# Optimization experiments

Hardware: AMD Instinct MI355X
Metric: run time of the kernel (lower is better)

The kernel has to match this reference:

```python
import jax, jax.numpy as jnp
import numpy as np

D_MODEL = 1024
HIDDEN = 2048            # hidden_dimension // num_smaller_experts_per_expert
E_ROUTED = 14            # total_num_experts*num_smaller - num_shared
E_SHARED = 2
TOP_K = 2                # num_activated*num_smaller - num_shared
EPS = 1e-9               # config.epsilon
RMS_EPS = 1.1920929e-07  # torch RMSNorm default eps=None -> finfo(float32).eps


def setup_inputs() -> dict:
    key = jax.random.key(0)
    ks = jax.random.split(key, 9)
    B, T = 2, 1024
    x = jax.random.normal(ks[0], (B, T, D_MODEL), dtype=jnp.float32)
    router_w = jax.random.normal(ks[1], (D_MODEL, E_ROUTED), dtype=jnp.float32) * 0.006
    rms_w = jnp.ones((E_ROUTED, D_MODEL), dtype=jnp.float32)
    w1 = jax.random.normal(ks[2], (E_ROUTED, D_MODEL, HIDDEN), dtype=jnp.float32) * 0.02
    w2 = jax.random.normal(ks[3], (E_ROUTED, HIDDEN, D_MODEL), dtype=jnp.float32) * 0.02
    rms_w_s = jnp.ones((E_SHARED, D_MODEL), dtype=jnp.float32)
    w1_s = jax.random.normal(ks[4], (E_SHARED, D_MODEL, HIDDEN), dtype=jnp.float32) * 0.02
    w2_s = jax.random.normal(ks[5], (E_SHARED, HIDDEN, D_MODEL), dtype=jnp.float32) * 0.02
    return {"x": x, "router_w": router_w, "rms_w": rms_w, "w1": w1, "w2": w2,
            "rms_w_s": rms_w_s, "w1_s": w1_s, "w2_s": w2_s}


def _ffn(xn, rw, W1, W2):
    # RMSNorm -> Linear -> SiLU -> Linear (dropout is identity in eval)
    ms = jnp.mean(xn * xn, axis=-1, keepdims=True)
    h = (xn * jax.lax.rsqrt(ms + RMS_EPS)) * rw
    return jax.nn.silu(h @ W1) @ W2


def reference(x, router_w, rms_w, w1, w2, rms_w_s, w1_s, w2_s):
    B, T, D = x.shape
    N = B * T
    xf = x.reshape(N, D)
    # router gates + top-k sparsification + renormalization
    gates = jax.nn.softmax(xf @ router_w, axis=-1)          # [N, E]
    top_v, top_i = jax.lax.top_k(gates, TOP_K)              # [N, K]
    masked = jnp.zeros_like(gates).at[jnp.arange(N)[:, None], top_i].set(top_v)
    masked = masked / (masked.sum(axis=-1, keepdims=True) + EPS)  # [N, E]
    # routed experts: compute each expert on all tokens, combine with sparse gate weights
    # (same math as dispatch/index_add combine since masked is 0 off the top-k)
    routed = jax.vmap(lambda rw_, W1_, W2_: _ffn(xf, rw_, W1_, W2_))(rms_w, w1, w2)  # [E, N, D]
    routed_out = jnp.einsum('end,ne->nd', routed, masked)
    # shared experts: unweighted sum
    shared = jax.vmap(lambda rw_, W1_, W2_: _ffn(xf, rw_, W1_, W2_))(rms_w_s, w1_s, w2_s).sum(0)
    return (routed_out + shared).reshape(B, T, D)
```

## Files before the change

kernel.cpp:

```cpp
#include <hip/hip_runtime.h>
#include <hip/hip_bf16.h>
#include <cstdint>
#include <cstddef>

#define D_MODEL 1024
#define HIDDEN 2048
#define E_ROUTED 14
#define E_TOT 16
#define NTOK 2048
#define NASSIGN 4096
#define NROWS 8192

typedef __bf16 bf16x8 __attribute__((ext_vector_type(8)));
typedef float f32x4 __attribute__((ext_vector_type(4)));

static __device__ __forceinline__ unsigned short f2b(float f) {
  unsigned int u = __builtin_bit_cast(unsigned int, f);
  u += 0x7fffu + ((u >> 16) & 1u);
  return (unsigned short)(u >> 16);
}

#define ASYNC_COPY16(gptr, lptr)                                                        \
  __builtin_amdgcn_global_load_lds(                                                     \
      (const __attribute__((address_space(1))) unsigned int*)(gptr),                    \
      (__attribute__((address_space(3))) unsigned int*)(lptr), 16, 0, 0)

__global__ __launch_bounds__(256) void router_kernel(
    const float* __restrict__ x, const float* __restrict__ rweight,
    int* __restrict__ topi, float* __restrict__ topw,
    unsigned short* __restrict__ xhat) {
  int n = blockIdx.x, tid = threadIdx.x;
  const float4 xv = reinterpret_cast<const float4*>(x + (size_t)n * D_MODEL)[tid];
  float ss = xv.x * xv.x + xv.y * xv.y + xv.z * xv.z + xv.w * xv.w;
  float lg[E_ROUTED];
#pragma unroll
  for (int e = 0; e < E_ROUTED; ++e) lg[e] = 0.f;
  const float xa[4] = {xv.x, xv.y, xv.z, xv.w};
#pragma unroll
  for (int i = 0; i < 4; ++i) {
    const float* rw = rweight + (size_t)(tid * 4 + i) * E_ROUTED;
    float xd = xa[i];
#pragma unroll
    for (int e = 0; e < E_ROUTED; ++e) lg[e] = fmaf(xd, rw[e], lg[e]);
  }
#pragma unroll
  for (int off = 32; off > 0; off >>= 1) {
    ss += __shfl_xor(ss, off);
#pragma unroll
    for (int e = 0; e < E_ROUTED; ++e) lg[e] += __shfl_xor(lg[e], off);
  }
  __shared__ float red[4][16];
  int wid = tid >> 6, lane = tid & 63;
  if (lane == 0) {
    red[wid][0] = ss;
#pragma unroll
    for (int e = 0; e < E_ROUTED; ++e) red[wid][1 + e] = lg[e];
  }
  __syncthreads();
  __shared__ float s_scale;
  if (tid == 0) {
    float fin[15];
    for (int v = 0; v < 15; ++v) fin[v] = red[0][v] + red[1][v] + red[2][v] + red[3][v];
    s_scale = rsqrtf(fin[0] * (1.f / D_MODEL) + 1.1920929e-07f);
    float mx = fin[1];
    for (int e = 1; e < E_ROUTED; ++e) mx = fmaxf(mx, fin[1 + e]);
    float p[E_ROUTED]; float Z = 0.f;
    for (int e = 0; e < E_ROUTED; ++e) { p[e] = __expf(fin[1 + e] - mx); Z += p[e]; }
    int i0 = 0; float v0 = p[0];
    for (int e = 1; e < E_ROUTED; ++e) if (p[e] > v0) { v0 = p[e]; i0 = e; }
    int i1 = (i0 == 0) ? 1 : 0; float v1 = p[i1];
    for (int e = 0; e < E_ROUTED; ++e) if (e != i0 && p[e] > v1) { v1 = p[e]; i1 = e; }
    v0 /= Z; v1 /= Z;
    float inv = 1.f / (v0 + v1 + 1e-9f);
    topi[2 * n] = i0; topi[2 * n + 1] = i1;
    topw[2 * n] = v0 * inv; topw[2 * n + 1] = v1 * inv;
  }
  __syncthreads();
  float sc = s_scale;
  ushort4 hx;
  hx.x = f2b(xv.x * sc); hx.y = f2b(xv.y * sc);
  hx.z = f2b(xv.z * sc); hx.w = f2b(xv.w * sc);
  reinterpret_cast<ushort4*>(xhat + (size_t)n * D_MODEL)[tid] = hx;
}

__global__ __launch_bounds__(256) void count_kernel(const int* __restrict__ topi,
                                                    int* __restrict__ goff,
                                                    int* __restrict__ cursor) {
  __shared__ int cnt[E_ROUTED];
  int tid = threadIdx.x;
  if (tid < E_ROUTED) cnt[tid] = 0;
  __syncthreads();
  for (int i = tid; i < NASSIGN; i += 256) atomicAdd(&cnt[topi[i]], 1);
  __syncthreads();
  if (tid == 0) {
    int acc = 0;
    for (int e = 0; e < E_ROUTED; ++e) { goff[e] = acc; cursor[e] = acc; acc += cnt[e]; }
    goff[E_ROUTED] = acc;
  }
}

__global__ __launch_bounds__(256) void scatter_kernel(
    const int* __restrict__ topi, const float* __restrict__ topw,
    int* __restrict__ cursor, int* __restrict__ row_token,
    float* __restrict__ row_gate, int* __restrict__ token_rows) {
  int i = blockIdx.x * 256 + threadIdx.x;
  if (i >= NASSIGN) return;
  int e = topi[i];
  int pos = atomicAdd(&cursor[e], 1);
  row_token[pos] = i >> 1;
  row_gate[pos] = topw[i];
  token_rows[i] = pos;
}

template <int K, int N, bool SCALE>
__global__ __launch_bounds__(256) void convT_kernel(
    const float* __restrict__ Wr, const float* __restrict__ Ws,
    const float* __restrict__ RWr, const float* __restrict__ RWs,
    unsigned short* __restrict__ outT) {
  __shared__ float tile[64][65];
  int g = blockIdx.z;
  const float* src = (g < E_ROUTED) ? Wr + (size_t)g * K * N
                                    : Ws + (size_t)(g - E_ROUTED) * K * N;
  const float* rw = nullptr;
  if constexpr (SCALE)
    rw = (g < E_ROUTED) ? RWr + (size_t)g * K : RWs + (size_t)(g - E_ROUTED) * K;
  int k0 = blockIdx.y * 64, nn0 = blockIdx.x * 64;
  int t = threadIdx.x;
  int kk = t >> 4, nc = (t & 15) * 4;
#pragma unroll
  for (int j = 0; j < 4; ++j) {
    int k = kk + j * 16;
    float4 v = *(const float4*)(src + (size_t)(k0 + k) * N + nn0 + nc);
    float s = 1.f;
    if constexpr (SCALE) s = rw[k0 + k];
    tile[k][nc]     = v.x * s;
    tile[k][nc + 1] = v.y * s;
    tile[k][nc + 2] = v.z * s;
    tile[k][nc + 3] = v.w * s;
  }
  __syncthreads();
  int k8 = (t & 7) * 8;
#pragma unroll
  for (int p = 0; p < 2; ++p) {
    int n = (t >> 3) + p * 32;
    uint4 pk;
    pk.x = (unsigned)f2b(tile[k8 + 0][n]) | ((unsigned)f2b(tile[k8 + 1][n]) << 16);
    pk.y = (unsigned)f2b(tile[k8 + 2][n]) | ((unsigned)f2b(tile[k8 + 3][n]) << 16);
    pk.z = (unsigned)f2b(tile[k8 + 4][n]) | ((unsigned)f2b(tile[k8 + 5][n]) << 16);
    pk.w = (unsigned)f2b(tile[k8 + 6][n]) | ((unsigned)f2b(tile[k8 + 7][n]) << 16);
    *(uint4*)(outT + ((size_t)g * N + nn0 + n) * K + k0 + k8) = pk;
  }
}

template <bool G1, int KTOT, int NTOT>
__global__ __launch_bounds__(256, 2) void ffn_gemm(
    const int* __restrict__ goff, const int* __restrict__ row_token,
    const float* __restrict__ row_gate,
    const unsigned short* __restrict__ Abase,
    const unsigned short* __restrict__ Wt,
    unsigned short* __restrict__ Hout, float* __restrict__ Yout) {
  int g = blockIdx.z;
  int grpStart, cnt;
  if (g < E_ROUTED) { grpStart = goff[g]; cnt = goff[g + 1] - goff[g]; }
  else { grpStart = NASSIGN + (g - E_ROUTED) * NTOK; cnt = NTOK; }
  int m0 = blockIdx.y * 128;
  if (m0 >= cnt) return;
  int n0 = blockIdx.x * 128;

  __shared__ __align__(16) char smem[2][32 * 1024];

  int tid = threadIdx.x, lane = tid & 63, wid = tid >> 6;
  int wr = (wid >> 1) * 64, wc = (wid & 1) * 64;
  int lrow = lane >> 3;
  int swz = lrow << 4;
  int colB = ((lane & 7) << 4) ^ swz;

  const char* aSrc[4];
  const char* bSrc[4];
#pragma unroll
  for (int i = 0; i < 4; ++i) {
    int row = wid * 32 + i * 8 + lrow;
    int rIdx = m0 + row; if (rIdx >= cnt) rIdx = cnt - 1;
    int srcRow;
    if constexpr (G1) srcRow = (g < E_ROUTED) ? row_token[grpStart + rIdx] : rIdx;
    else srcRow = grpStart + rIdx;
    aSrc[i] = (const char*)(Abase + (size_t)srcRow * KTOT) + colB;
    bSrc[i] = (const char*)(Wt + ((size_t)g * NTOT + n0 + row) * KTOT) + colB;
  }

  f32x4 acc[4][4];
#pragma unroll
  for (int m = 0; m < 4; ++m)
#pragma unroll
    for (int n = 0; n < 4; ++n)
#pragma unroll
      for (int c = 0; c < 4; ++c) acc[m][n][c] = 0.f;

  auto STAGE = [&](int buf) {
    char* sA = smem[buf];
    char* sB = smem[buf] + 16 * 1024;
#pragma unroll
    for (int i = 0; i < 4; ++i) ASYNC_COPY16(aSrc[i], sA + wid * 4096 + i * 1024);
#pragma unroll
    for (int i = 0; i < 4; ++i) ASYNC_COPY16(bSrc[i], sB + wid * 4096 + i * 1024);
#pragma unroll
    for (int i = 0; i < 4; ++i) { aSrc[i] += 128; bSrc[i] += 128; }
  };
  auto COMPUTE = [&](int buf) {
    const char* sA = smem[buf];
    const char* sB = smem[buf] + 16 * 1024;
#pragma unroll
    for (int ks = 0; ks < 2; ++ks) {
      int kb = ks * 64 + ((lane >> 4) << 4);
      bf16x8 af[4], bfr[4];
#pragma unroll
      for (int m = 0; m < 4; ++m) {
        int r = wr + m * 16 + (lane & 15);
        af[m] = *(const bf16x8*)(sA + (r << 7) + (kb ^ ((r & 7) << 4)));
      }
#pragma unroll
      for (int n = 0; n < 4; ++n) {
        int r = wc + n * 16 + (lane & 15);
        bfr[n] = *(const bf16x8*)(sB + (r << 7) + (kb ^ ((r & 7) << 4)));
      }
#pragma unroll
      for (int m = 0; m < 4; ++m)
#pragma unroll
        for (int n = 0; n < 4; ++n)
          acc[m][n] = __builtin_amdgcn_mfma_f32_16x16x32_bf16(af[m], bfr[n], acc[m][n], 0, 0, 0);
    }
  };

  constexpr int NT = KTOT / 64;
  STAGE(0);
  __syncthreads();
  for (int kt = 0; kt < NT; kt += 2) {
    STAGE(1);
    COMPUTE(0);
    __syncthreads();
    if (kt + 2 < NT) STAGE(0);
    COMPUTE(1);
    __syncthreads();
  }

  int lr = (lane >> 4) * 4, lc = lane & 15;
#pragma unroll
  for (int m = 0; m < 4; ++m) {
    int rloc = m0 + wr + m * 16 + lr;
#pragma unroll
    for (int j = 0; j < 4; ++j) {
      if (rloc + j < cnt) {
        size_t r = (size_t)(grpStart + rloc + j);
        if constexpr (G1) {
#pragma unroll
          for (int n = 0; n < 4; ++n) {
            float v = acc[m][n][j];
            float sv = v / (1.f + __expf(-v));
            Hout[r * HIDDEN + (n0 + wc + n * 16 + lc)] = f2b(sv);
          }
        } else {
          float gate = 1.f;
          if (g < E_ROUTED) gate = row_gate[r];
#pragma unroll
          for (int n = 0; n < 4; ++n)
            Yout[r * D_MODEL + (n0 + wc + n * 16 + lc)] = acc[m][n][j] * gate;
        }
      }
    }
  }
}

__global__ __launch_bounds__(256) void combine_kernel(
    const float* __restrict__ y, const int* __restrict__ token_rows,
    float* __restrict__ out) {
  int n = blockIdx.x, tid = threadIdx.x;
  int a0 = token_rows[2 * n], a1 = token_rows[2 * n + 1];
  const float4* y0 = reinterpret_cast<const float4*>(y + (size_t)a0 * D_MODEL);
  const float4* y1 = reinterpret_cast<const float4*>(y + (size_t)a1 * D_MODEL);
  const float4* s0 = reinterpret_cast<const float4*>(y + (size_t)(NASSIGN + n) * D_MODEL);
  const float4* s1 = reinterpret_cast<const float4*>(y + (size_t)(NASSIGN + NTOK + n) * D_MODEL);
  float4 a = y0[tid], b = y1[tid], c = s0[tid], d = s1[tid];
  float4 r;
  r.x = a.x + b.x + c.x + d.x;
  r.y = a.y + b.y + c.y + d.y;
  r.z = a.z + b.z + c.z + d.z;
  r.w = a.w + b.w + c.w + d.w;
  reinterpret_cast<float4*>(out + (size_t)n * D_MODEL)[tid] = r;
}

extern "C" void kernel_launch(void* const* d_in, const int* in_sizes, int n_in,
                              void* d_out, int out_size, void* d_ws, size_t ws_size,
                              hipStream_t stream) {
  const float* x        = (const float*)d_in[0];
  const float* router_w = (const float*)d_in[1];
  const float* rms_w    = (const float*)d_in[2];
  const float* w1       = (const float*)d_in[3];
  const float* w2       = (const float*)d_in[4];
  const float* rms_w_s  = (const float*)d_in[5];
  const float* w1_s     = (const float*)d_in[6];
  const float* w2_s     = (const float*)d_in[7];
  float* out = (float*)d_out;

  char* ws = (char*)d_ws;
  unsigned short* xhat = (unsigned short*)ws;
  unsigned short* h    = (unsigned short*)(ws + ((size_t)4 << 20));
  float* y             = (float*)(ws + ((size_t)36 << 20));
  unsigned short* w1t  = (unsigned short*)(ws + ((size_t)68 << 20));
  unsigned short* w2t  = (unsigned short*)(ws + ((size_t)132 << 20));
  char* meta = ws + ((size_t)196 << 20);
  int*   topi       = (int*)(meta);
  float* topw       = (float*)(meta + (16 << 10));
  int*   row_token  = (int*)(meta + (32 << 10));
  float* row_gate   = (float*)(meta + (48 << 10));
  int*   token_rows = (int*)(meta + (64 << 10));
  int*   goff       = (int*)(meta + (80 << 10));
  int*   cursor     = (int*)(meta + (80 << 10) + 256);

  router_kernel<<<NTOK, 256, 0, stream>>>(x, router_w, topi, topw, xhat);
  count_kernel<<<1, 256, 0, stream>>>(topi, goff, cursor);
  scatter_kernel<<<NASSIGN / 256, 256, 0, stream>>>(topi, topw, cursor, row_token,
                                                    row_gate, token_rows);
  convT_kernel<D_MODEL, HIDDEN, true><<<dim3(HIDDEN / 64, D_MODEL / 64, E_TOT), 256, 0, stream>>>(
      w1, w1_s, rms_w, rms_w_s, w1t);
  convT_kernel<HIDDEN, D_MODEL, false><<<dim3(D_MODEL / 64, HIDDEN / 64, E_TOT), 256, 0, stream>>>(
      w2, w2_s, nullptr, nullptr, w2t);
  ffn_gemm<true, D_MODEL, HIDDEN><<<dim3(HIDDEN / 128, 16, E_TOT), 256, 0, stream>>>(
      goff, row_token, row_gate, xhat, w1t, h, nullptr);
  ffn_gemm<false, HIDDEN, D_MODEL><<<dim3(D_MODEL / 128, 16, E_TOT), 256, 0, stream>>>(
      goff, row_token, row_gate, h, w2t, nullptr, y);
  combine_kernel<<<NTOK, 256, 0, stream>>>(y, token_rows, out);
}
```

Baseline: 251.8 us.

## Use 256x256 GEMM tiles with 512 threads, split-K on second GEMM, barrier-based pipeline

The grouped FFN GEMM moves from 128x128 tiles with 256 threads to 256x256 tiles with 512 threads and 64KB of LDS per stage. The K loop is rewritten as a two-stage async pipeline using explicit vmcnt waits, raw s_barrier and setprio. MFMA work is skipped on m-fragments that lie past the group's row count. Shared experts are scheduled first in the grid. The second GEMM splits K in two and writes two partial outputs, which the combine kernel sums. This aims for more data reuse per tile and better load/compute overlap, at the cost of a doubled y buffer, more LDS per block (possibly lower occupancy) and more wasted work on partial tiles.

```diff
diff --git a/kernel.cpp b/kernel.cpp
--- a/kernel.cpp
+++ b/kernel.cpp
@@ -152,118 +152,129 @@
   }
 }
 
-template <bool G1, int KTOT, int NTOT>
-__global__ __launch_bounds__(256, 2) void ffn_gemm(
+template <bool G1, int KTOT, int NTOT, int KSL>
+__global__ __launch_bounds__(512, 2) void ffn_gemm(
     const int* __restrict__ goff, const int* __restrict__ row_token,
     const float* __restrict__ row_gate,
     const unsigned short* __restrict__ Abase,
     const unsigned short* __restrict__ Wt,
     unsigned short* __restrict__ Hout, float* __restrict__ Yout) {
-  int g = blockIdx.z;
+  constexpr int KLEN = KTOT / KSL;
+  constexpr int NT = KLEN / 64;
+
+  int bz = blockIdx.z;
+  int g = (bz < 2) ? (E_ROUTED + bz) : (bz - 2);
   int grpStart, cnt;
   if (g < E_ROUTED) { grpStart = goff[g]; cnt = goff[g + 1] - goff[g]; }
   else { grpStart = NASSIGN + (g - E_ROUTED) * NTOK; cnt = NTOK; }
-  int m0 = blockIdx.y * 128;
+  int m0 = blockIdx.x * 256;
   if (m0 >= cnt) return;
-  int n0 = blockIdx.x * 128;
-
-  __shared__ __align__(16) char smem[2][32 * 1024];
-
-  int tid = threadIdx.x, lane = tid & 63, wid = tid >> 6;
-  int wr = (wid >> 1) * 64, wc = (wid & 1) * 64;
-  int lrow = lane >> 3;
-  int swz = lrow << 4;
-  int colB = ((lane & 7) << 4) ^ swz;
-
+  int yb = blockIdx.y, ks = 0;
+  if constexpr (KSL > 1) { ks = yb >> 2; yb &= 3; }
+  int n0 = yb * 256;
+  int kOff = ks * KLEN;
+
+  __shared__ __align__(16) char smem[2][64 * 1024];
+
+  int t = threadIdx.x, lane = t & 63, wid = t >> 6;
+  int wm = wid >> 2, wn = wid & 3;
+  int mlocal = cnt - m0 - wm * 128;
+
+  int colB = ((t & 7) << 4) ^ (((t >> 3) & 7) << 4);
   const char* aSrc[4];
   const char* bSrc[4];
 #pragma unroll
   for (int i = 0; i < 4; ++i) {
-    int row = wid * 32 + i * 8 + lrow;
+    int row = i * 64 + (t >> 3);
     int rIdx = m0 + row; if (rIdx >= cnt) rIdx = cnt - 1;
     int srcRow;
     if constexpr (G1) srcRow = (g < E_ROUTED) ? row_token[grpStart + rIdx] : rIdx;
     else srcRow = grpStart + rIdx;
-    aSrc[i] = (const char*)(Abase + (size_t)srcRow * KTOT) + colB;
-    bSrc[i] = (const char*)(Wt + ((size_t)g * NTOT + n0 + row) * KTOT) + colB;
-  }
-
-  f32x4 acc[4][4];
-#pragma unroll
-  for (int m = 0; m < 4; ++m)
+    aSrc[i] = (const char*)(Abase + (size_t)srcRow * KTOT + kOff) + colB;
+    bSrc[i] = (const char*)(Wt + ((size_t)g * NTOT + n0 + row) * KTOT + kOff) + colB;
+  }
+
+  f32x4 acc[8][4];
+#pragma unroll
+  for (int m = 0; m < 8; ++m)
 #pragma unroll
     for (int n = 0; n < 4; ++n)
 #pragma unroll
       for (int c = 0; c < 4; ++c) acc[m][n][c] = 0.f;
 
   auto STAGE = [&](int buf) {
-    char* sA = smem[buf];
-    char* sB = smem[buf] + 16 * 1024;
-#pragma unroll
-    for (int i = 0; i < 4; ++i) ASYNC_COPY16(aSrc[i], sA + wid * 4096 + i * 1024);
-#pragma unroll
-    for (int i = 0; i < 4; ++i) ASYNC_COPY16(bSrc[i], sB + wid * 4096 + i * 1024);
+    char* base = smem[buf];
+#pragma unroll
+    for (int i = 0; i < 4; ++i) ASYNC_COPY16(aSrc[i], base + i * 8192 + wid * 1024);
+#pragma unroll
+    for (int i = 0; i < 4; ++i) ASYNC_COPY16(bSrc[i], base + 32768 + i * 8192 + wid * 1024);
 #pragma unroll
     for (int i = 0; i < 4; ++i) { aSrc[i] += 128; bSrc[i] += 128; }
   };
   auto COMPUTE = [&](int buf) {
     const char* sA = smem[buf];
-    const char* sB = smem[buf] + 16 * 1024;
-#pragma unroll
-    for (int ks = 0; ks < 2; ++ks) {
-      int kb = ks * 64 + ((lane >> 4) << 4);
-      bf16x8 af[4], bfr[4];
-#pragma unroll
-      for (int m = 0; m < 4; ++m) {
-        int r = wr + m * 16 + (lane & 15);
-        af[m] = *(const bf16x8*)(sA + (r << 7) + (kb ^ ((r & 7) << 4)));
+    const char* sB = smem[buf] + 32768;
+    int l15 = lane & 15, lk = (lane >> 4) << 4;
+#pragma unroll
+    for (int ksp = 0; ksp < 2; ++ksp) {
+      int kb = ksp * 64 + lk;
+      bf16x8 bfr[4];
+#pragma unroll
+      for (int nf = 0; nf < 4; ++nf) {
+        int r = wn * 64 + nf * 16 + l15;
+        bfr[nf] = *(const bf16x8*)(sB + (r << 7) + (kb ^ ((r & 7) << 4)));
       }
 #pragma unroll
-      for (int n = 0; n < 4; ++n) {
-        int r = wc + n * 16 + (lane & 15);
-        bfr[n] = *(const bf16x8*)(sB + (r << 7) + (kb ^ ((r & 7) << 4)));
+      for (int mf = 0; mf < 8; ++mf) {
+        if (mf * 16 < mlocal) {
+          int r = wm * 128 + mf * 16 + l15;
+          bf16x8 a = *(const bf16x8*)(sA + (r << 7) + (kb ^ ((r & 7) << 4)));
+#pragma unroll
+          for (int nf = 0; nf < 4; ++nf)
+            acc[mf][nf] = __builtin_amdgcn_mfma_f32_16x16x32_bf16(a, bfr[nf], acc[mf][nf], 0, 0, 0);
+        }
       }
-#pragma unroll
-      for (int m = 0; m < 4; ++m)
-#pragma unroll
-        for (int n = 0; n < 4; ++n)
-          acc[m][n] = __builtin_amdgcn_mfma_f32_16x16x32_bf16(af[m], bfr[n], acc[m][n], 0, 0, 0);
     }
   };
 
-  constexpr int NT = KTOT / 64;
   STAGE(0);
-  __syncthreads();
-  for (int kt = 0; kt < NT; kt += 2) {
-    STAGE(1);
-    COMPUTE(0);
-    __syncthreads();
-    if (kt + 2 < NT) STAGE(0);
-    COMPUTE(1);
-    __syncthreads();
+  STAGE(1);
+  for (int kt = 0; kt < NT; ++kt) {
+    if (kt < NT - 1) asm volatile("s_waitcnt vmcnt(8)" ::: "memory");
+    else             asm volatile("s_waitcnt vmcnt(0)" ::: "memory");
+    __builtin_amdgcn_s_barrier();
+    __builtin_amdgcn_sched_barrier(0);
+    __builtin_amdgcn_s_setprio(1);
+    COMPUTE(kt & 1);
+    __builtin_amdgcn_s_setprio(0);
+    __builtin_amdgcn_s_barrier();
+    __builtin_amdgcn_sched_barrier(0);
+    if (kt + 2 < NT) STAGE(kt & 1);
   }
 
   int lr = (lane >> 4) * 4, lc = lane & 15;
 #pragma unroll
-  for (int m = 0; m < 4; ++m) {
-    int rloc = m0 + wr + m * 16 + lr;
+  for (int mf = 0; mf < 8; ++mf) {
+    if (mf * 16 >= mlocal) continue;
+    int rloc = m0 + wm * 128 + mf * 16 + lr;
 #pragma unroll
     for (int j = 0; j < 4; ++j) {
       if (rloc + j < cnt) {
         size_t r = (size_t)(grpStart + rloc + j);
         if constexpr (G1) {
 #pragma unroll
-          for (int n = 0; n < 4; ++n) {
-            float v = acc[m][n][j];
+          for (int nf = 0; nf < 4; ++nf) {
+            float v = acc[mf][nf][j];
             float sv = v / (1.f + __expf(-v));
-            Hout[r * HIDDEN + (n0 + wc + n * 16 + lc)] = f2b(sv);
+            Hout[r * HIDDEN + (n0 + wn * 64 + nf * 16 + lc)] = f2b(sv);
           }
         } else {
           float gate = 1.f;
           if (g < E_ROUTED) gate = row_gate[r];
-#pragma unroll
-          for (int n = 0; n < 4; ++n)
-            Yout[r * D_MODEL + (n0 + wc + n * 16 + lc)] = acc[m][n][j] * gate;
+          float* yo = Yout + (size_t)ks * NROWS * D_MODEL;
+#pragma unroll
+          for (int nf = 0; nf < 4; ++nf)
+            yo[r * D_MODEL + (n0 + wn * 64 + nf * 16 + lc)] = acc[mf][nf][j] * gate;
         }
       }
     }
@@ -275,16 +286,19 @@
     float* __restrict__ out) {
   int n = blockIdx.x, tid = threadIdx.x;
   int a0 = token_rows[2 * n], a1 = token_rows[2 * n + 1];
-  const float4* y0 = reinterpret_cast<const float4*>(y + (size_t)a0 * D_MODEL);
-  const float4* y1 = reinterpret_cast<const float4*>(y + (size_t)a1 * D_MODEL);
-  const float4* s0 = reinterpret_cast<const float4*>(y + (size_t)(NASSIGN + n) * D_MODEL);
-  const float4* s1 = reinterpret_cast<const float4*>(y + (size_t)(NASSIGN + NTOK + n) * D_MODEL);
-  float4 a = y0[tid], b = y1[tid], c = s0[tid], d = s1[tid];
-  float4 r;
-  r.x = a.x + b.x + c.x + d.x;
-  r.y = a.y + b.y + c.y + d.y;
-  r.z = a.z + b.z + c.z + d.z;
-  r.w = a.w + b.w + c.w + d.w;
+  float4 r = {0.f, 0.f, 0.f, 0.f};
+#pragma unroll
+  for (int ks = 0; ks < 2; ++ks) {
+    const float* yb = y + (size_t)ks * NROWS * D_MODEL;
+    float4 a = reinterpret_cast<const float4*>(yb + (size_t)a0 * D_MODEL)[tid];
+    float4 b = reinterpret_cast<const float4*>(yb + (size_t)a1 * D_MODEL)[tid];
+    float4 c = reinterpret_cast<const float4*>(yb + (size_t)(NASSIGN + n) * D_MODEL)[tid];
+    float4 d = reinterpret_cast<const float4*>(yb + (size_t)(NASSIGN + NTOK + n) * D_MODEL)[tid];
+    r.x += a.x + b.x + c.x + d.x;
+    r.y += a.y + b.y + c.y + d.y;
+    r.z += a.z + b.z + c.z + d.z;
+    r.w += a.w + b.w + c.w + d.w;
+  }
   reinterpret_cast<float4*>(out + (size_t)n * D_MODEL)[tid] = r;
 }
 
@@ -324,9 +338,9 @@
       w1, w1_s, rms_w, rms_w_s, w1t);
   convT_kernel<HIDDEN, D_MODEL, false><<<dim3(D_MODEL / 64, HIDDEN / 64, E_TOT), 256, 0, stream>>>(
       w2, w2_s, nullptr, nullptr, w2t);
-  ffn_gemm<true, D_MODEL, HIDDEN><<<dim3(HIDDEN / 128, 16, E_TOT), 256, 0, stream>>>(
+  ffn_gemm<true, D_MODEL, HIDDEN, 1><<<dim3(16, 8, E_TOT), 512, 0, stream>>>(
       goff, row_token, row_gate, xhat, w1t, h, nullptr);
-  ffn_gemm<false, HIDDEN, D_MODEL><<<dim3(D_MODEL / 128, 16, E_TOT), 256, 0, stream>>>(
+  ffn_gemm<false, HIDDEN, D_MODEL, 2><<<dim3(16, 8, E_TOT), 512, 0, stream>>>(
       goff, row_token, row_gate, h, w2t, nullptr, y);
   combine_kernel<<<NTOK, 256, 0, stream>>>(y, token_rows, out);
 }
```

New measurement: 683.4 us. 171% more time.
